# Optimization experiments

Hardware: AMD Instinct MI355X
Metric: run time of the kernel (lower is better)

Reference implementation:

```python
import jax, jax.numpy as jnp
import numpy as np

B, T, D, H = 4, 2048, 1024, 16
DH = D // H  # 64


def setup_inputs() -> dict:
    key = jax.random.key(0)
    k1, k2, k3 = jax.random.split(key, 3)
    x = jax.random.normal(k1, (B, T, D), dtype=jnp.float32)
    w_qkv = jax.random.normal(k2, (D, 3 * D), dtype=jnp.float32) * (D ** -0.5)
    w_out = jax.random.normal(k3, (D, D), dtype=jnp.float32) * (D ** -0.5)
    return {"x": x, "w_qkv": w_qkv, "w_out": w_out}


def reference(x, w_qkv, w_out):
    b, t, d = x.shape
    qkv = jnp.einsum('btd,de->bte', x, w_qkv)  # [B,T,3D]
    q, k, v = jnp.split(qkv, 3, axis=-1)
    # [B,H,T,DH]
    q = q.reshape(b, t, H, DH).transpose(0, 2, 1, 3)
    k = k.reshape(b, t, H, DH).transpose(0, 2, 1, 3)
    v = v.reshape(b, t, H, DH).transpose(0, 2, 1, 3)
    logits = jnp.einsum('bhqd,bhkd->bhqk', q, k) * (1.0 / jnp.sqrt(jnp.float32(DH)))
    # causal bias: -inf strictly above the diagonal (key index > query index)
    causal = jnp.tril(jnp.ones((t, t), dtype=bool))
    logits = jnp.where(causal, logits, jnp.float32(-jnp.inf))
    scores = jax.nn.softmax(logits, axis=-1)
    y = jnp.einsum('bhqk,bhkd->bhqd', scores, v)
    y = y.transpose(0, 2, 1, 3).reshape(b, t, d)
    return jnp.einsum('btd,de->bte', y, w_out)
```

## Files before the change

kernel.cpp:

```cpp
#include <hip/hip_runtime.h>
#include <hip/hip_bf16.h>


namespace {
constexpr int kB = 4, kT = 2048, kD = 1024, kH = 16;
constexpr int kM = kB * kT;
constexpr int kNq = 3 * kD;
constexpr float kS = 0.180336880f;
}

typedef unsigned short u16;
typedef short bf16x8 __attribute__((ext_vector_type(8)));
typedef float f32x4 __attribute__((ext_vector_type(4)));

__device__ __forceinline__ u16 f2bf(float f) {
  unsigned int u = __float_as_uint(f);
  u += 0x7fffu + ((u >> 16) & 1u);
  return (u16)(u >> 16);
}
__device__ __forceinline__ unsigned int pack2(float a, float b) {
  return (unsigned int)f2bf(a) | ((unsigned int)f2bf(b) << 16);
}
__device__ __forceinline__ unsigned int cvtpk(float a, float b) {
  unsigned int r;
  asm("v_cvt_pk_bf16_f32 %0, %1, %2" : "=v"(r) : "v"(a), "v"(b));
  return r;
}

__device__ __forceinline__ void gload16(const u16* g, u16* l) {
  __builtin_amdgcn_global_load_lds(
      (const __attribute__((address_space(1))) unsigned int*)(uintptr_t)g,
      (__attribute__((address_space(3))) unsigned int*)(uintptr_t)l, 16, 0, 0);
}

__global__ __launch_bounds__(256) void cvt_bf16(const float* __restrict__ x,
                                                u16* __restrict__ xb) {
  const size_t i = ((size_t)blockIdx.x * 256 + threadIdx.x) * 8;
  const float4 v0 = *(const float4*)(x + i);
  const float4 v1 = *(const float4*)(x + i + 4);
  uint4 p;
  p.x = pack2(v0.x, v0.y);
  p.y = pack2(v0.z, v0.w);
  p.z = pack2(v1.x, v1.y);
  p.w = pack2(v1.z, v1.w);
  *(uint4*)(xb + i) = p;
}

__global__ __launch_bounds__(256) void transpose_bf(const float* __restrict__ W,
                                                    u16* __restrict__ WT,
                                                    int K, int N, int nscale) {
  __shared__ float T[32][33];
  const int tid = threadIdx.x;
  const int nb = blockIdx.x * 32, kb = blockIdx.y * 32;
  const int r = tid >> 3, c = (tid & 7) * 4;
  const float4 v = *(const float4*)&W[(size_t)(kb + r) * N + nb + c];
  T[r][c + 0] = v.x;
  T[r][c + 1] = v.y;
  T[r][c + 2] = v.z;
  T[r][c + 3] = v.w;
  __syncthreads();
  const float s = (nb + r < nscale) ? kS : 1.0f;
  uint2 p;
  p.x = pack2(T[c + 0][r] * s, T[c + 1][r] * s);
  p.y = pack2(T[c + 2][r] * s, T[c + 3][r] * s);
  *(uint2*)&WT[(size_t)(nb + r) * K + kb + c] = p;
}

__global__ __launch_bounds__(512, 2) void gemm256(const u16* __restrict__ A,
                                                  const u16* __restrict__ BT,
                                                  u16* __restrict__ C, int lda,
                                                  int ldc) {
  __shared__ u16 As[2][256 * 64];
  __shared__ u16 Bs[2][256 * 64];
  constexpr int NT = kD / 64;
  const int tid = threadIdx.x;
  const int wid = tid >> 6, lane = tid & 63;
  const int col = lane & 15, quad = lane >> 4;
  const int wm_ = wid >> 2, wn_ = wid & 3;

  const int nwg = gridDim.x * gridDim.y;
  int flat = blockIdx.y * gridDim.x + blockIdx.x;
  flat = (flat & 7) * (nwg >> 3) + (flat >> 3);
  const int n0 = (flat % gridDim.x) * 256;
  const int m0 = (flat / gridDim.x) * 256;

  const int srow = tid >> 3;
  const int scol8 = (tid & 7) * 8;
  const int gch8 = ((tid & 7) ^ (srow & 7)) * 8;
  const u16* const Ag = A + (size_t)(m0 + srow) * lda + gch8;
  const u16* const Bg = BT + (size_t)(n0 + srow) * kD + gch8;

  f32x4 acc[8][4];
#pragma unroll
  for (int i = 0; i < 8; ++i)
#pragma unroll
    for (int j = 0; j < 4; ++j) acc[i][j] = (f32x4){0.f, 0.f, 0.f, 0.f};

#define STAGE_A(buf, rbase, k0)                                              \
  do {                                                                       \
    gload16(Ag + (size_t)(rbase)*lda + (k0),                                 \
            &As[buf][((rbase) + srow) * 64 + scol8]);                        \
    gload16(Ag + (size_t)((rbase) + 64) * lda + (k0),                        \
            &As[buf][((rbase) + 64 + srow) * 64 + scol8]);                   \
  } while (0)
#define STAGE_B(buf, rbase, k0)                                              \
  do {                                                                       \
    gload16(Bg + (size_t)(rbase)*kD + (k0),                                  \
            &Bs[buf][((rbase) + srow) * 64 + scol8]);                        \
    gload16(Bg + (size_t)((rbase) + 64) * kD + (k0),                         \
            &Bs[buf][((rbase) + 64 + srow) * 64 + scol8]);                   \
  } while (0)

  STAGE_A(0, 0, 0);
  STAGE_B(0, 0, 0);
  STAGE_B(0, 128, 0);
  STAGE_A(0, 128, 0);
  STAGE_A(1, 0, 64);
  STAGE_B(1, 0, 64);
  asm volatile("s_waitcnt vmcnt(4)" ::: "memory");
  __builtin_amdgcn_s_barrier();

  int cur = 0;
  for (int t = 0; t < NT; ++t) {
    const int nxt = cur ^ 1;
#pragma unroll
    for (int ph = 0; ph < 4; ++ph) {
      const int mq = ph >> 1, nq = ph & 1;
      bf16x8 af[4][2], bv[2][2];
#pragma unroll
      for (int mi = 0; mi < 4; ++mi) {
        const int r = mq * 128 + wm_ * 64 + mi * 16 + col;
#pragma unroll
        for (int ks = 0; ks < 2; ++ks)
          af[mi][ks] = *(const bf16x8*)&As[cur][r * 64 +
                                               (((ks * 4 + quad) ^ (r & 7)) *
                                                8)];
      }
#pragma unroll
      for (int ni = 0; ni < 2; ++ni) {
        const int r = nq * 128 + wn_ * 32 + ni * 16 + col;
#pragma unroll
        for (int ks = 0; ks < 2; ++ks)
          bv[ni][ks] = *(const bf16x8*)&Bs[cur][r * 64 +
                                               (((ks * 4 + quad) ^ (r & 7)) *
                                                8)];
      }
      if (ph == 0) {
        if (t + 1 < NT) STAGE_B(nxt, 128, (t + 1) * 64);
      } else if (ph == 1) {
        if (t + 1 < NT) STAGE_A(nxt, 128, (t + 1) * 64);
      } else if (ph == 2) {
        if (t + 2 < NT) STAGE_A(cur, 0, (t + 2) * 64);
      } else {
        if (t + 2 < NT) STAGE_B(cur, 0, (t + 2) * 64);
      }
      __builtin_amdgcn_s_barrier();
      asm volatile("s_waitcnt lgkmcnt(0)" ::: "memory");
      __builtin_amdgcn_s_setprio(1);
#pragma unroll
      for (int mi = 0; mi < 4; ++mi)
#pragma unroll
        for (int ni = 0; ni < 2; ++ni)
#pragma unroll
          for (int ks = 0; ks < 2; ++ks)
            acc[mq * 4 + mi][nq * 2 + ni] =
                __builtin_amdgcn_mfma_f32_16x16x32_bf16(
                    af[mi][ks], bv[ni][ks], acc[mq * 4 + mi][nq * 2 + ni], 0,
                    0, 0);
      __builtin_amdgcn_s_setprio(0);
      if (ph == 3) {
        if (t + 2 < NT)
          asm volatile("s_waitcnt vmcnt(4)" ::: "memory");
        else if (t + 1 < NT)
          asm volatile("s_waitcnt vmcnt(0)" ::: "memory");
      }
      __builtin_amdgcn_s_barrier();
    }
    cur = nxt;
  }
#undef STAGE_A
#undef STAGE_B

#pragma unroll
  for (int mig = 0; mig < 8; ++mig) {
    const int row =
        m0 + (mig >> 2) * 128 + wm_ * 64 + (mig & 3) * 16 + quad * 4;
#pragma unroll
    for (int reg = 0; reg < 4; ++reg) {
      u16* cp = C + (size_t)(row + reg) * ldc;
#pragma unroll
      for (int nig = 0; nig < 4; ++nig) {
        const int cc = n0 + (nig >> 1) * 128 + wn_ * 32 + (nig & 1) * 16 + col;
        cp[cc] = f2bf(acc[mig][nig][reg]);
      }
    }
  }
}

template <bool F32OUT>
__global__ __launch_bounds__(256) void gemm_bt(const u16* __restrict__ A,
                                               const u16* __restrict__ BT,
                                               void* __restrict__ Cv, int lda,
                                               int ldc) {
  __shared__ u16 As[128 * 32];
  __shared__ u16 Bs[128 * 32];
  const int tid = threadIdx.x;
  const int w = tid >> 6, lane = tid & 63;
  const int col = lane & 15, quad = lane >> 4;
  const int wm = (w & 1) * 64, wn = (w >> 1) * 64;
  const int m0 = blockIdx.y * 128, n0 = blockIdx.x * 128;

  const int s0 = tid, s1 = 256 + tid;
  const int ar0 = s0 >> 2, ak0 = ((s0 & 3) ^ ((ar0 >> 1) & 3)) * 8;
  const int ar1 = s1 >> 2, ak1 = ((s1 & 3) ^ ((ar1 >> 1) & 3)) * 8;
  const u16* agp0 = A + (size_t)(m0 + ar0) * lda + ak0;
  const u16* agp1 = A + (size_t)(m0 + ar1) * lda + ak1;
  const u16* bgp0 = BT + (size_t)(n0 + ar0) * kD + ak0;
  const u16* bgp1 = BT + (size_t)(n0 + ar1) * kD + ak1;
  u16* al0 = &As[s0 * 8];
  u16* al1 = &As[s1 * 8];
  u16* bl0 = &Bs[s0 * 8];
  u16* bl1 = &Bs[s1 * 8];

  f32x4 acc[4][4];
#pragma unroll
  for (int mi = 0; mi < 4; ++mi)
#pragma unroll
    for (int ni = 0; ni < 4; ++ni) acc[mi][ni] = (f32x4){0.f, 0.f, 0.f, 0.f};

  for (int k0 = 0; k0 < kD; k0 += 32) {
    __syncthreads();
    gload16(agp0 + k0, al0);
    gload16(agp1 + k0, al1);
    gload16(bgp0 + k0, bl0);
    gload16(bgp1 + k0, bl1);
    __syncthreads();
    bf16x8 af[4], bfr[4];
#pragma unroll
    for (int mi = 0; mi < 4; ++mi) {
      const int r = wm + mi * 16 + col;
      af[mi] = *(const bf16x8*)&As[r * 32 + ((quad ^ ((r >> 1) & 3)) * 8)];
    }
#pragma unroll
    for (int ni = 0; ni < 4; ++ni) {
      const int r = wn + ni * 16 + col;
      bfr[ni] = *(const bf16x8*)&Bs[r * 32 + ((quad ^ ((r >> 1) & 3)) * 8)];
    }
#pragma unroll
    for (int mi = 0; mi < 4; ++mi)
#pragma unroll
      for (int ni = 0; ni < 4; ++ni)
        acc[mi][ni] = __builtin_amdgcn_mfma_f32_16x16x32_bf16(
            af[mi], bfr[ni], acc[mi][ni], 0, 0, 0);
  }

#pragma unroll
  for (int mi = 0; mi < 4; ++mi)
#pragma unroll
    for (int reg = 0; reg < 4; ++reg) {
      const int row = m0 + wm + mi * 16 + quad * 4 + reg;
#pragma unroll
      for (int ni = 0; ni < 4; ++ni) {
        const int cc = n0 + wn + ni * 16 + col;
        if (F32OUT)
          ((float*)Cv)[(size_t)row * ldc + cc] = acc[mi][ni][reg];
        else
          ((u16*)Cv)[(size_t)row * ldc + cc] = f2bf(acc[mi][ni][reg]);
      }
    }
}

__global__ __launch_bounds__(256) void attn_fwd(u16* __restrict__ qkv) {
  __shared__ u16 Ks[2][64 * 64];
  __shared__ u16 Vt[64][72];
  __shared__ u16 Ps[64][72];
  const int tid = threadIdx.x;
  const int w = tid >> 6, lane = tid & 63;
  const int col = lane & 15, quad = lane >> 4;
  const int bh = blockIdx.x;
  const int b = bh >> 4, h = bh & 15;
  const int pa = blockIdx.y;
  const size_t base = (size_t)(b * kT) * kNq + h * 64;

  const int krr = lane >> 3;
  const int ksw = (lane & 7) ^ krr;
  const u16* const kgbase =
      qkv + base + kD + (size_t)(w * 16 + krr) * kNq + ksw * 8;

  const int vkp = (tid & 31) * 2, vd0 = (tid >> 5) * 8;
  const u16* const vgbase = qkv + base + 2 * kD + (size_t)vkp * kNq + vd0;

  bf16x8 onesf;
#pragma unroll
  for (int i = 0; i < 8; ++i) onesf[i] = (short)0x3F80;

  int cur = 0;
#pragma unroll
  for (int pass = 0; pass < 2; ++pass) {
    const int qt = pass ? (31 - pa) : pa;
    const int q0 = qt << 6;

    bf16x8 aq[2];
#pragma unroll
    for (int ks = 0; ks < 2; ++ks)
      aq[ks] = *(const bf16x8*)(qkv + base + (size_t)(q0 + w * 16 + col) * kNq +
                                ks * 32 + quad * 8);

    gload16(kgbase, &Ks[cur][(w * 16) * 64]);
    gload16(kgbase + (size_t)8 * kNq, &Ks[cur][(w * 16 + 8) * 64]);
    uint4 va = *(const uint4*)vgbase;
    uint4 vb = *(const uint4*)(vgbase + kNq);

    f32x4 o[4];
#pragma unroll
    for (int nt = 0; nt < 4; ++nt) o[nt] = (f32x4){0.f, 0.f, 0.f, 0.f};
    f32x4 o4 = (f32x4){0.f, 0.f, 0.f, 0.f};

    for (int kt = 0; kt <= qt; ++kt) {
      __syncthreads();
      {
        const unsigned int* aw = (const unsigned int*)&va;
        const unsigned int* bw = (const unsigned int*)&vb;
#pragma unroll
        for (int i = 0; i < 4; ++i) {
          *(unsigned int*)&Vt[vd0 + 2 * i][vkp] =
              __builtin_amdgcn_perm(bw[i], aw[i], 0x05040100u);
          *(unsigned int*)&Vt[vd0 + 2 * i + 1][vkp] =
              __builtin_amdgcn_perm(bw[i], aw[i], 0x07060302u);
        }
      }
      __syncthreads();

      if (kt < qt) {
        const size_t ko = (size_t)((kt + 1) << 6) * kNq;
        gload16(kgbase + ko, &Ks[cur ^ 1][(w * 16) * 64]);
        gload16(kgbase + ko + (size_t)8 * kNq, &Ks[cur ^ 1][(w * 16 + 8) * 64]);
        va = *(const uint4*)(vgbase + ko);
        vb = *(const uint4*)(vgbase + ko + kNq);
      }

      f32x4 st[4];
#pragma unroll
      for (int nt = 0; nt < 4; ++nt) st[nt] = (f32x4){0.f, 0.f, 0.f, 0.f};
#pragma unroll
      for (int ks = 0; ks < 2; ++ks) {
#pragma unroll
        for (int nt = 0; nt < 4; ++nt) {
          const int kr = nt * 16 + col;
          const bf16x8 bk = *(const bf16x8*)&Ks[cur][kr * 64 +
                                                     (((ks * 4 + quad) ^
                                                       (col & 7)) *
                                                      8)];
          st[nt] = __builtin_amdgcn_mfma_f32_16x16x32_bf16(bk, aq[ks], st[nt],
                                                           0, 0, 0);
        }
      }

      if (kt == qt) {
        const int qrel = w * 16 + col;
#pragma unroll
        for (int nt = 0; nt < 4; ++nt)
#pragma unroll
          for (int reg = 0; reg < 4; ++reg) {
            const int krel = nt * 16 + quad * 4 + reg;
            st[nt][reg] =
                (krel <= qrel) ? __builtin_amdgcn_exp2f(st[nt][reg]) : 0.f;
          }
      } else {
#pragma unroll
        for (int nt = 0; nt < 4; ++nt)
#pragma unroll
          for (int reg = 0; reg < 4; ++reg)
            st[nt][reg] = __builtin_amdgcn_exp2f(st[nt][reg]);
      }

#pragma unroll
      for (int nt = 0; nt < 4; ++nt) {
        uint2 pk;
        pk.x = cvtpk(st[nt][0], st[nt][1]);
        pk.y = cvtpk(st[nt][2], st[nt][3]);
        *(uint2*)&Ps[w * 16 + col][nt * 16 + quad * 4] = pk;
      }

#pragma unroll
      for (int ks = 0; ks < 2; ++ks) {
        const bf16x8 ap =
            *(const bf16x8*)&Ps[w * 16 + col][ks * 32 + quad * 8];
#pragma unroll
        for (int nt = 0; nt < 4; ++nt) {
          const bf16x8 bv =
              *(const bf16x8*)&Vt[nt * 16 + col][ks * 32 + quad * 8];
          o[nt] = __builtin_amdgcn_mfma_f32_16x16x32_bf16(ap, bv, o[nt], 0, 0,
                                                          0);
        }
        o4 = __builtin_amdgcn_mfma_f32_16x16x32_bf16(ap, onesf, o4, 0, 0, 0);
      }
      cur ^= 1;
    }

#pragma unroll
    for (int reg = 0; reg < 4; ++reg) {
      const float inv = 1.0f / o4[reg];
      u16* yp = qkv + base + (size_t)(q0 + w * 16 + quad * 4 + reg) * kNq;
#pragma unroll
      for (int nt = 0; nt < 4; ++nt)
        yp[nt * 16 + col] = f2bf(o[nt][reg] * inv);
    }
  }
}

extern "C" void kernel_launch(void* const* d_in, const int* in_sizes, int n_in,
                              void* d_out, int out_size, void* d_ws,
                              size_t ws_size, hipStream_t stream) {
  const float* x = (const float*)d_in[0];
  const float* w_qkv = (const float*)d_in[1];
  const float* w_out = (const float*)d_in[2];

  u16* wqkvT = (u16*)d_ws;
  u16* woutT = wqkvT + (size_t)kNq * kD;
  u16* qkvb = woutT + (size_t)kD * kD;
  u16* xb = (u16*)d_out;

  cvt_bf16<<<kM * kD / 2048, 256, 0, stream>>>(x, xb);
  transpose_bf<<<dim3(kNq / 32, kD / 32), 256, 0, stream>>>(w_qkv, wqkvT, kD,
                                                            kNq, kD);
  transpose_bf<<<dim3(kD / 32, kD / 32), 256, 0, stream>>>(w_out, woutT, kD,
                                                           kD, 0);
  gemm256<<<dim3(kNq / 256, kM / 256), 512, 0, stream>>>(xb, wqkvT, qkvb, kD,
                                                         kNq);
  attn_fwd<<<dim3(kB * kH, 16), 256, 0, stream>>>(qkvb);
  gemm_bt<true><<<dim3(kD / 128, kM / 128), 256, 0, stream>>>(qkvb, woutT,
                                                              d_out, kNq, kD);
}
```

Measured before the change: 257.3 us.

## Reuse A/B register fragments across GEMM quadrant phases and deepen prefetch

```diff
diff --git a/kernel.cpp b/kernel.cpp
--- a/kernel.cpp
+++ b/kernel.cpp
@@ -66,6 +66,46 @@
   *(uint2*)&WT[(size_t)(nb + r) * K + kb + c] = p;
 }
 
+__device__ __forceinline__ void read_afrag(bf16x8 (&AF)[4][2], const u16* Asb,
+                                           int half, int wm_, int col,
+                                           int quad) {
+#pragma unroll
+  for (int mi = 0; mi < 4; ++mi) {
+    const int r = half * 128 + wm_ * 64 + mi * 16 + col;
+#pragma unroll
+    for (int ks = 0; ks < 2; ++ks)
+      AF[mi][ks] =
+          *(const bf16x8*)&Asb[r * 64 + (((ks * 4 + quad) ^ (r & 7)) * 8)];
+  }
+}
+__device__ __forceinline__ void read_bfrag(bf16x8 (&BV)[2][2], const u16* Bsb,
+                                           int half, int wn_, int col,
+                                           int quad) {
+#pragma unroll
+  for (int ni = 0; ni < 2; ++ni) {
+    const int r = half * 128 + wn_ * 32 + ni * 16 + col;
+#pragma unroll
+    for (int ks = 0; ks < 2; ++ks)
+      BV[ni][ks] =
+          *(const bf16x8*)&Bsb[r * 64 + (((ks * 4 + quad) ^ (r & 7)) * 8)];
+  }
+}
+template <int MQ, int NQ>
+__device__ __forceinline__ void mfma_quad(f32x4 (&acc)[8][4],
+                                          const bf16x8 (&AF)[4][2],
+                                          const bf16x8 (&BV)[2][2]) {
+#pragma unroll
+  for (int mi = 0; mi < 4; ++mi)
+#pragma unroll
+    for (int ni = 0; ni < 2; ++ni)
+#pragma unroll
+      for (int ks = 0; ks < 2; ++ks)
+        acc[MQ * 4 + mi][NQ * 2 + ni] =
+            __builtin_amdgcn_mfma_f32_16x16x32_bf16(
+                AF[mi][ks], BV[ni][ks], acc[MQ * 4 + mi][NQ * 2 + ni], 0, 0,
+                0);
+}
+
 __global__ __launch_bounds__(512, 2) void gemm256(const u16* __restrict__ A,
                                                   const u16* __restrict__ BT,
                                                   u16* __restrict__ C, int lda,
@@ -96,87 +136,76 @@
 #pragma unroll
     for (int j = 0; j < 4; ++j) acc[i][j] = (f32x4){0.f, 0.f, 0.f, 0.f};
 
-#define STAGE_A(buf, rbase, k0)                                              \
-  do {                                                                       \
-    gload16(Ag + (size_t)(rbase)*lda + (k0),                                 \
-            &As[buf][((rbase) + srow) * 64 + scol8]);                        \
-    gload16(Ag + (size_t)((rbase) + 64) * lda + (k0),                        \
-            &As[buf][((rbase) + 64 + srow) * 64 + scol8]);                   \
+#define STAGE_A(buf, half, k0)                                           \
+  do {                                                                   \
+    gload16(Ag + (size_t)((half)*128) * lda + (k0),                      \
+            &As[buf][((half)*128 + srow) * 64 + scol8]);                 \
+    gload16(Ag + (size_t)((half)*128 + 64) * lda + (k0),                 \
+            &As[buf][((half)*128 + 64 + srow) * 64 + scol8]);            \
   } while (0)
-#define STAGE_B(buf, rbase, k0)                                              \
-  do {                                                                       \
-    gload16(Bg + (size_t)(rbase)*kD + (k0),                                  \
-            &Bs[buf][((rbase) + srow) * 64 + scol8]);                        \
-    gload16(Bg + (size_t)((rbase) + 64) * kD + (k0),                         \
-            &Bs[buf][((rbase) + 64 + srow) * 64 + scol8]);                   \
+#define STAGE_B(buf, half, k0)                                           \
+  do {                                                                   \
+    gload16(Bg + (size_t)((half)*128) * kD + (k0),                       \
+            &Bs[buf][((half)*128 + srow) * 64 + scol8]);                 \
+    gload16(Bg + (size_t)((half)*128 + 64) * kD + (k0),                  \
+            &Bs[buf][((half)*128 + 64 + srow) * 64 + scol8]);            \
   } while (0)
 
   STAGE_A(0, 0, 0);
   STAGE_B(0, 0, 0);
-  STAGE_B(0, 128, 0);
-  STAGE_A(0, 128, 0);
+  STAGE_B(0, 1, 0);
+  STAGE_A(0, 1, 0);
   STAGE_A(1, 0, 64);
-  STAGE_B(1, 0, 64);
-  asm volatile("s_waitcnt vmcnt(4)" ::: "memory");
+  STAGE_B(1, 1, 64);
+  STAGE_A(1, 1, 64);
+  asm volatile("s_waitcnt vmcnt(6)" ::: "memory");
   __builtin_amdgcn_s_barrier();
 
-  int cur = 0;
   for (int t = 0; t < NT; ++t) {
-    const int nxt = cur ^ 1;
-#pragma unroll
-    for (int ph = 0; ph < 4; ++ph) {
-      const int mq = ph >> 1, nq = ph & 1;
-      bf16x8 af[4][2], bv[2][2];
-#pragma unroll
-      for (int mi = 0; mi < 4; ++mi) {
-        const int r = mq * 128 + wm_ * 64 + mi * 16 + col;
-#pragma unroll
-        for (int ks = 0; ks < 2; ++ks)
-          af[mi][ks] = *(const bf16x8*)&As[cur][r * 64 +
-                                               (((ks * 4 + quad) ^ (r & 7)) *
-                                                8)];
-      }
-#pragma unroll
-      for (int ni = 0; ni < 2; ++ni) {
-        const int r = nq * 128 + wn_ * 32 + ni * 16 + col;
-#pragma unroll
-        for (int ks = 0; ks < 2; ++ks)
-          bv[ni][ks] = *(const bf16x8*)&Bs[cur][r * 64 +
-                                               (((ks * 4 + quad) ^ (r & 7)) *
-                                                8)];
-      }
-      if (ph == 0) {
-        if (t + 1 < NT) STAGE_B(nxt, 128, (t + 1) * 64);
-      } else if (ph == 1) {
-        if (t + 1 < NT) STAGE_A(nxt, 128, (t + 1) * 64);
-      } else if (ph == 2) {
-        if (t + 2 < NT) STAGE_A(cur, 0, (t + 2) * 64);
-      } else {
-        if (t + 2 < NT) STAGE_B(cur, 0, (t + 2) * 64);
-      }
-      __builtin_amdgcn_s_barrier();
-      asm volatile("s_waitcnt lgkmcnt(0)" ::: "memory");
-      __builtin_amdgcn_s_setprio(1);
-#pragma unroll
-      for (int mi = 0; mi < 4; ++mi)
-#pragma unroll
-        for (int ni = 0; ni < 2; ++ni)
-#pragma unroll
-          for (int ks = 0; ks < 2; ++ks)
-            acc[mq * 4 + mi][nq * 2 + ni] =
-                __builtin_amdgcn_mfma_f32_16x16x32_bf16(
-                    af[mi][ks], bv[ni][ks], acc[mq * 4 + mi][nq * 2 + ni], 0,
-                    0, 0);
-      __builtin_amdgcn_s_setprio(0);
-      if (ph == 3) {
-        if (t + 2 < NT)
-          asm volatile("s_waitcnt vmcnt(4)" ::: "memory");
-        else if (t + 1 < NT)
-          asm volatile("s_waitcnt vmcnt(0)" ::: "memory");
-      }
-      __builtin_amdgcn_s_barrier();
-    }
-    cur = nxt;
+    const int cur = t & 1;
+    const u16* Ac = &As[cur][0];
+    const u16* Bc = &Bs[cur][0];
+    const int k2 = (t + 2) * 64;
+    bf16x8 af0[4][2], af1[4][2], bv0[2][2], bv1[2][2];
+
+    read_afrag(af0, Ac, 0, wm_, col, quad);
+    read_bfrag(bv0, Bc, 0, wn_, col, quad);
+    if (t + 1 < NT) STAGE_B(cur ^ 1, 0, (t + 1) * 64);
+    __builtin_amdgcn_s_barrier();
+    asm volatile("s_waitcnt lgkmcnt(0)" ::: "memory");
+    __builtin_amdgcn_s_setprio(1);
+    mfma_quad<0, 0>(acc, af0, bv0);
+    __builtin_amdgcn_s_setprio(0);
+    __builtin_amdgcn_s_barrier();
+
+    read_bfrag(bv1, Bc, 1, wn_, col, quad);
+    if (t + 2 < NT) STAGE_A(cur, 0, k2);
+    __builtin_amdgcn_s_barrier();
+    asm volatile("s_waitcnt lgkmcnt(0)" ::: "memory");
+    __builtin_amdgcn_s_setprio(1);
+    mfma_quad<0, 1>(acc, af0, bv1);
+    __builtin_amdgcn_s_setprio(0);
+    __builtin_amdgcn_s_barrier();
+
+    read_afrag(af1, Ac, 1, wm_, col, quad);
+    if (t + 2 < NT) STAGE_B(cur, 1, k2);
+    __builtin_amdgcn_s_barrier();
+    asm volatile("s_waitcnt lgkmcnt(0)" ::: "memory");
+    __builtin_amdgcn_s_setprio(1);
+    mfma_quad<1, 0>(acc, af1, bv0);
+    __builtin_amdgcn_s_setprio(0);
+    __builtin_amdgcn_s_barrier();
+
+    if (t + 2 < NT) STAGE_A(cur, 1, k2);
+    __builtin_amdgcn_s_barrier();
+    __builtin_amdgcn_s_setprio(1);
+    mfma_quad<1, 1>(acc, af1, bv1);
+    __builtin_amdgcn_s_setprio(0);
+    if (t + 2 < NT)
+      asm volatile("s_waitcnt vmcnt(6)" ::: "memory");
+    else if (t + 1 < NT)
+      asm volatile("s_waitcnt vmcnt(0)" ::: "memory");
+    __builtin_amdgcn_s_barrier();
   }
 #undef STAGE_A
 #undef STAGE_B
```

New measurement: 248.8 us. 1.03x faster.
